# Optimization experiments

Hardware: AMD Instinct MI355X
Metric: run time of the kernel (lower is better)

## Reference

```python
import jax, jax.numpy as jnp
import numpy as np

N_NODES = 100000


def _graph_conv(x, W, b, src, dst, deg_out, deg_in, relu):
    # DGL GraphConv, norm='both':
    #   h = (x * D_out^{-1/2}) W ; agg = scatter_sum over edges ; out = agg * D_in^{-1/2} + b
    norm_src = jax.lax.rsqrt(jnp.maximum(deg_out, 1.0))  # [N]
    norm_dst = jax.lax.rsqrt(jnp.maximum(deg_in, 1.0))   # [N]
    h = (x * norm_src[:, None]) @ W                       # [N, d_out]
    agg = jax.ops.segment_sum(h[src], dst, num_segments=N_NODES)  # [N, d_out]
    out = agg * norm_dst[:, None] + b
    return jax.nn.relu(out) if relu else out


def setup_inputs() -> dict:
    key = jax.random.key(0)
    ks = jax.random.split(key, 8)
    E = 1600000
    in_dim, hid_dim, out_dim = 128, 128, 64
    feat = jax.random.normal(ks[0], (N_NODES, in_dim), dtype=jnp.float32)
    edge_index = jax.random.randint(ks[1], (2, E), 0, N_NODES, dtype=jnp.int64)
    s = 1.0 / np.sqrt(in_dim)
    sh = 1.0 / np.sqrt(hid_dim)
    return {
        "feat": feat,
        "edge_index": edge_index,
        "W0": jax.random.normal(ks[2], (in_dim, hid_dim), dtype=jnp.float32) * s,
        "b0": jnp.zeros((hid_dim,), dtype=jnp.float32),
        "W1": jax.random.normal(ks[3], (hid_dim, hid_dim), dtype=jnp.float32) * sh,
        "b1": jnp.zeros((hid_dim,), dtype=jnp.float32),
        "W2": jax.random.normal(ks[4], (hid_dim, out_dim), dtype=jnp.float32) * sh,
        "b2": jnp.zeros((out_dim,), dtype=jnp.float32),
    }


def reference(feat, edge_index, W0, b0, W1, b1, W2, b2):
    src, dst = edge_index[0], edge_index[1]
    ones = jnp.ones(src.shape, dtype=feat.dtype)
    deg_out = jax.ops.segment_sum(ones, src, num_segments=N_NODES)  # src out-degree
    deg_in = jax.ops.segment_sum(ones, dst, num_segments=N_NODES)   # dst in-degree
    h = _graph_conv(feat, W0, b0, src, dst, deg_out, deg_in, relu=True)
    h = _graph_conv(h, W1, b1, src, dst, deg_out, deg_in, relu=True)
    h = _graph_conv(h, W2, b2, src, dst, deg_out, deg_in, relu=False)
    return h
```

## Files before the change

kernel.cpp:

```cpp
#include <hip/hip_runtime.h>
#include <hip/hip_fp16.h>


typedef _Float16 h8 __attribute__((ext_vector_type(8)));
typedef float f32x4 __attribute__((ext_vector_type(4)));

#define HWORDS 25024
#define NHS 64
#define NHD 256

__global__ __launch_bounds__(1024) void k_pre(const int* __restrict__ src,
                                              const int* __restrict__ dst, int E,
                                              unsigned* __restrict__ histo_s,
                                              unsigned* __restrict__ histo_d,
                                              const float* __restrict__ W0,
                                              const float* __restrict__ W1,
                                              const float* __restrict__ W2,
                                              __half* __restrict__ Wt0,
                                              __half* __restrict__ Wt1,
                                              __half* __restrict__ Wt2) {
    __shared__ unsigned H[HWORDS];
    const int b = blockIdx.x;
    const int tid = threadIdx.x;
    if (b < NHS + NHD) {
        const bool isS = b < NHS;
        const int c = isS ? b : b - NHS;
        const int NC = isS ? NHS : NHD;
        const int* arr = isS ? src : dst;
        unsigned* outp = (isS ? histo_s : histo_d) + (size_t)c * HWORDS;
        for (int i = tid; i < HWORDS; i += 1024) H[i] = 0;
        __syncthreads();
        const int perB = ((E + NC - 1) / NC + 3) & ~3;
        const int e0 = min(c * perB, E), e1 = min(e0 + perB, E);
        int i = e0 + tid * 4;
        for (; i + 3 < e1; i += 4096) {
            int4 s4 = *(const int4*)(arr + i);
            atomicAdd(&H[s4.x >> 2], 1u << ((s4.x & 3) * 8));
            atomicAdd(&H[s4.y >> 2], 1u << ((s4.y & 3) * 8));
            atomicAdd(&H[s4.z >> 2], 1u << ((s4.z & 3) * 8));
            atomicAdd(&H[s4.w >> 2], 1u << ((s4.w & 3) * 8));
        }
        for (; i < e1; ++i) {
            int s = arr[i];
            atomicAdd(&H[s >> 2], 1u << ((s & 3) * 8));
        }
        __syncthreads();
        for (int i2 = tid; i2 < HWORDS; i2 += 1024) outp[i2] = H[i2];
    } else {
        for (int j = tid; j < 40960; j += 1024) {
            if (j < 16384) {
                int nn = j >> 7, k = j & 127;
                Wt0[j] = __float2half(W0[k * 128 + nn]);
            } else if (j < 32768) {
                int i2 = j - 16384;
                int nn = i2 >> 7, k = i2 & 127;
                Wt1[i2] = __float2half(W1[k * 128 + nn]);
            } else {
                int i2 = j - 32768;
                int nn = i2 >> 7, k = i2 & 127;
                Wt2[i2] = __float2half(W2[k * 64 + nn]);
            }
        }
    }
}

__global__ __launch_bounds__(256) void k_scan1(const unsigned* __restrict__ histo_s,
                                               unsigned* __restrict__ histo_d,
                                               int* __restrict__ rp,
                                               int* __restrict__ bsum,
                                               float* __restrict__ ns,
                                               float* __restrict__ nd, int n) {
    __shared__ unsigned qsd[4][64];
    __shared__ unsigned qss[4][64];
    __shared__ unsigned di4[64];
    __shared__ unsigned do4[64];
    const int tid = threadIdx.x, lane = tid & 63, q = tid >> 6;
    const int w = blockIdx.x * 64 + lane;
    {
        unsigned s = 0;
#pragma unroll 8
        for (int b = q * (NHD / 4); b < (q + 1) * (NHD / 4); ++b)
            s += histo_d[(size_t)b * HWORDS + w];
        qsd[q][lane] = s;
        unsigned s2 = 0;
#pragma unroll
        for (int b = q * (NHS / 4); b < (q + 1) * (NHS / 4); ++b)
            s2 += histo_s[(size_t)b * HWORDS + w];
        qss[q][lane] = s2;
    }
    __syncthreads();
    if (q == 0) {
        di4[lane] = qsd[0][lane] + qsd[1][lane] + qsd[2][lane] + qsd[3][lane];
        do4[lane] = qss[0][lane] + qss[1][lane] + qss[2][lane] + qss[3][lane];
    }
    {
        unsigned run = 0;
        for (int k = 0; k < q; ++k) run += qsd[k][lane];
#pragma unroll 8
        for (int b = q * (NHD / 4); b < (q + 1) * (NHD / 4); ++b) {
            unsigned c4 = histo_d[(size_t)b * HWORDS + w];
            histo_d[(size_t)b * HWORDS + w] = run;
            run += c4;
        }
    }
    __syncthreads();
    int i = blockIdx.x * 256 + tid;
    int v = 0;
    if (i < n) {
        int sh = (tid & 3) * 8;
        v = (di4[tid >> 2] >> sh) & 255;
        int dgo = (do4[tid >> 2] >> sh) & 255;
        nd[i] = rsqrtf((float)max(v, 1));
        ns[i] = rsqrtf((float)max(dgo, 1));
    }
    int x = v;
#pragma unroll
    for (int off = 1; off < 64; off <<= 1) {
        int t = __shfl_up(x, off, 64);
        if (lane >= off) x += t;
    }
    __shared__ int ws[4];
    if (lane == 63) ws[q] = x;
    __syncthreads();
    int wo = 0;
    for (int k = 0; k < q; ++k) wo += ws[k];
    int incl = wo + x;
    if (i < n) rp[i] = incl - v;
    if (tid == 255) bsum[blockIdx.x] = incl;
}

__global__ __launch_bounds__(512) void k_scan2(int* __restrict__ bsum, int nb,
                                               int* __restrict__ rpN) {
    __shared__ int s[512];
    const int tid = threadIdx.x;
    int v = (tid < nb) ? bsum[tid] : 0;
    s[tid] = v;
    __syncthreads();
    for (int off = 1; off < 512; off <<= 1) {
        int t = (tid >= off) ? s[tid - off] : 0;
        __syncthreads();
        s[tid] += t;
        __syncthreads();
    }
    if (tid < nb) bsum[tid] = s[tid] - v;
    if (tid == nb - 1) *rpN = v;
}

__global__ __launch_bounds__(1024) void k_scatter2(const int* __restrict__ src,
                                                   const int* __restrict__ dst, int E,
                                                   const int* __restrict__ rp,
                                                   const int* __restrict__ bsum,
                                                   const unsigned* __restrict__ pfx_all,
                                                   int* __restrict__ csr) {
    __shared__ unsigned Hd[HWORDS];
    const int tid = threadIdx.x;
    for (int i = tid; i < HWORDS; i += 1024) Hd[i] = 0;
    __syncthreads();
    const int c = blockIdx.x;
    const int perB = ((E + NHD - 1) / NHD + 3) & ~3;
    const int e0 = min(c * perB, E), e1 = min(e0 + perB, E);
    const unsigned* pfx = pfx_all + (size_t)c * HWORDS;
    int i = e0 + tid * 4;
    for (; i + 3 < e1; i += 4096) {
        int4 d4 = *(const int4*)(dst + i);
        int4 s4 = *(const int4*)(src + i);
#define PROC(dd, ss)                                                            \
        {                                                                       \
            int sh = ((dd) & 3) * 8;                                            \
            int base = rp[dd] + bsum[(dd) >> 8] +                               \
                       (int)((pfx[(dd) >> 2] >> sh) & 255u);                    \
            unsigned old = atomicAdd(&Hd[(dd) >> 2], 1u << sh);                 \
            csr[base + (int)((old >> sh) & 255u)] = (ss);                       \
        }
        PROC(d4.x, s4.x) PROC(d4.y, s4.y) PROC(d4.z, s4.z) PROC(d4.w, s4.w)
    }
    for (; i < e1; ++i) PROC(dst[i], src[i])
#undef PROC
}

template <int BN, bool F32A>
__device__ __forceinline__ void gemm_body(const void* __restrict__ Ap,
                                          const __half* __restrict__ Wt,
                                          __half* __restrict__ C, int n, int gb) {
    constexpr int K = 128, BM = 128, LDR = K + 8;
    __shared__ __half Al[BM * LDR];
    __shared__ __half Bl[BN * LDR];
    const int tid = threadIdx.x;
    const int row0 = gb * BM;
    if (F32A) {
        const float* A = (const float*)Ap;
#pragma unroll
        for (int q = 0; q < 16; ++q) {
            int fi = q * 256 + tid;
            int r = fi >> 5, c = (fi & 31) * 4;
            int gr = row0 + r;
            float4 v = make_float4(0.f, 0.f, 0.f, 0.f);
            if (gr < n) v = *(const float4*)(A + (size_t)gr * K + c);
            __half2 h0 = __floats2half2_rn(v.x, v.y);
            __half2 h1 = __floats2half2_rn(v.z, v.w);
            uint2 pk = make_uint2(*(unsigned*)&h0, *(unsigned*)&h1);
            *(uint2*)&Al[r * LDR + c] = pk;
        }
    } else {
        const __half* A = (const __half*)Ap;
#pragma unroll
        for (int q = 0; q < 8; ++q) {
            int fi = q * 256 + tid;
            int r = fi >> 4, c = (fi & 15) * 8;
            int gr = row0 + r;
            float4 v = make_float4(0.f, 0.f, 0.f, 0.f);
            if (gr < n) v = *(const float4*)(A + (size_t)gr * K + c);
            *(float4*)&Al[r * LDR + c] = v;
        }
    }
#pragma unroll
    for (int q = 0; q < BN / 16; ++q) {
        int fi = q * 256 + tid;
        int r = fi >> 4, c = (fi & 15) * 8;
        *(float4*)&Bl[r * LDR + c] = *(const float4*)(Wt + (size_t)r * K + c);
    }
    __syncthreads();
    const int wid = tid >> 6, lane = tid & 63;
    const int lo = lane & 15, hi = lane >> 4;
    constexpr int NC = BN / 16;
    f32x4 acc[2][NC];
#pragma unroll
    for (int t = 0; t < 2; ++t)
#pragma unroll
        for (int c = 0; c < NC; ++c) acc[t][c] = (f32x4){0.f, 0.f, 0.f, 0.f};
#pragma unroll
    for (int kc = 0; kc < 4; ++kc) {
        h8 aF[2];
#pragma unroll
        for (int t = 0; t < 2; ++t)
            aF[t] = *(const h8*)&Al[(32 * wid + 16 * t + lo) * LDR + 32 * kc + 8 * hi];
#pragma unroll
        for (int c = 0; c < NC; ++c) {
            h8 bF = *(const h8*)&Bl[(16 * c + lo) * LDR + 32 * kc + 8 * hi];
#pragma unroll
            for (int t = 0; t < 2; ++t)
                acc[t][c] = __builtin_amdgcn_mfma_f32_16x16x32_f16(aF[t], bF, acc[t][c], 0, 0, 0);
        }
    }
#pragma unroll
    for (int t = 0; t < 2; ++t) {
#pragma unroll
        for (int j = 0; j < 4; ++j) {
            int gr = row0 + 32 * wid + 16 * t + 4 * hi + j;
            if (gr < n) {
#pragma unroll
                for (int c = 0; c < NC; ++c)
                    C[(size_t)gr * BN + 16 * c + lo] = __float2half(acc[t][c][j]);
            }
        }
    }
}

template <int BN, bool F32A>
__global__ __launch_bounds__(256) void k_gemm(const void* __restrict__ A,
                                              const __half* __restrict__ Wt,
                                              __half* __restrict__ C, int n) {
    gemm_body<BN, F32A>(A, Wt, C, n, blockIdx.x);
}

template <bool RELU, bool SSCALE>
__global__ __launch_bounds__(256) void k_agg128h(const __half2* __restrict__ H,
                                                 const int* __restrict__ rp,
                                                 const int* __restrict__ bsum,
                                                 const int* __restrict__ cs,
                                                 const float* __restrict__ nd,
                                                 const float* __restrict__ ns,
                                                 const float* __restrict__ b,
                                                 __half2* __restrict__ out, int n) {
    const int wid = threadIdx.x >> 6, lane = threadIdx.x & 63;
    const int node = blockIdx.x * 4 + wid;
    if (node >= n) return;
    const int beg = rp[node] + bsum[node >> 8];
    const int end = rp[node + 1] + bsum[(node + 1) >> 8];
    float2 a0 = make_float2(0.f, 0.f), a1 = a0, a2 = a0, a3 = a0;
    float2 a4 = a0, a5 = a0, a6 = a0, a7 = a0;
    for (int e = beg; e < end; e += 8) {
        int s[8];
        float w[8];
#pragma unroll
        for (int j = 0; j < 8; ++j) {
            int idx = e + j;
            int r = (idx < end) ? idx : beg;
            r = __builtin_amdgcn_readfirstlane(r);
            s[j] = cs[r];
            w[j] = (idx < end) ? 1.f : 0.f;
        }
        if (SSCALE) {
#pragma unroll
            for (int j = 0; j < 8; ++j) w[j] *= ns[s[j]];
        }
        float2 v0 = __half22float2(H[(size_t)s[0] * 64 + lane]);
        float2 v1 = __half22float2(H[(size_t)s[1] * 64 + lane]);
        float2 v2 = __half22float2(H[(size_t)s[2] * 64 + lane]);
        float2 v3 = __half22float2(H[(size_t)s[3] * 64 + lane]);
        float2 v4 = __half22float2(H[(size_t)s[4] * 64 + lane]);
        float2 v5 = __half22float2(H[(size_t)s[5] * 64 + lane]);
        float2 v6 = __half22float2(H[(size_t)s[6] * 64 + lane]);
        float2 v7 = __half22float2(H[(size_t)s[7] * 64 + lane]);
        a0.x = fmaf(v0.x, w[0], a0.x); a0.y = fmaf(v0.y, w[0], a0.y);
        a1.x = fmaf(v1.x, w[1], a1.x); a1.y = fmaf(v1.y, w[1], a1.y);
        a2.x = fmaf(v2.x, w[2], a2.x); a2.y = fmaf(v2.y, w[2], a2.y);
        a3.x = fmaf(v3.x, w[3], a3.x); a3.y = fmaf(v3.y, w[3], a3.y);
        a4.x = fmaf(v4.x, w[4], a4.x); a4.y = fmaf(v4.y, w[4], a4.y);
        a5.x = fmaf(v5.x, w[5], a5.x); a5.y = fmaf(v5.y, w[5], a5.y);
        a6.x = fmaf(v6.x, w[6], a6.x); a6.y = fmaf(v6.y, w[6], a6.y);
        a7.x = fmaf(v7.x, w[7], a7.x); a7.y = fmaf(v7.y, w[7], a7.y);
    }
    const float sc = nd[node];
    const float sn = ns[node];
    float2 bb = ((const float2*)b)[lane];
    float ax = ((a0.x + a1.x) + (a2.x + a3.x)) + ((a4.x + a5.x) + (a6.x + a7.x));
    float ay = ((a0.y + a1.y) + (a2.y + a3.y)) + ((a4.y + a5.y) + (a6.y + a7.y));
    float ox = ax * sc + bb.x;
    float oy = ay * sc + bb.y;
    if (RELU) { ox = fmaxf(ox, 0.f); oy = fmaxf(oy, 0.f); }
    ox *= sn; oy *= sn;
    out[(size_t)node * 64 + lane] = __floats2half2_rn(ox, oy);
}

__global__ __launch_bounds__(256) void k_agg64h(const __half* __restrict__ H,
                                                const int* __restrict__ rp,
                                                const int* __restrict__ bsum,
                                                const int* __restrict__ cs,
                                                const float* __restrict__ nd,
                                                const float* __restrict__ b,
                                                float* __restrict__ out, int n) {
    const int wid = threadIdx.x >> 6, lane = threadIdx.x & 63;
    const int node = blockIdx.x * 4 + wid;
    if (node >= n) return;
    const int beg = rp[node] + bsum[node >> 8];
    const int end = rp[node + 1] + bsum[(node + 1) >> 8];
    float a0 = 0.f, a1 = 0.f, a2 = 0.f, a3 = 0.f;
    float a4 = 0.f, a5 = 0.f, a6 = 0.f, a7 = 0.f;
    for (int e = beg; e < end; e += 8) {
        int s[8];
        float w[8];
#pragma unroll
        for (int j = 0; j < 8; ++j) {
            int idx = e + j;
            int r = (idx < end) ? idx : beg;
            r = __builtin_amdgcn_readfirstlane(r);
            s[j] = cs[r];
            w[j] = (idx < end) ? 1.f : 0.f;
        }
        a0 = fmaf(__half2float(H[(size_t)s[0] * 64 + lane]), w[0], a0);
        a1 = fmaf(__half2float(H[(size_t)s[1] * 64 + lane]), w[1], a1);
        a2 = fmaf(__half2float(H[(size_t)s[2] * 64 + lane]), w[2], a2);
        a3 = fmaf(__half2float(H[(size_t)s[3] * 64 + lane]), w[3], a3);
        a4 = fmaf(__half2float(H[(size_t)s[4] * 64 + lane]), w[4], a4);
        a5 = fmaf(__half2float(H[(size_t)s[5] * 64 + lane]), w[5], a5);
        a6 = fmaf(__half2float(H[(size_t)s[6] * 64 + lane]), w[6], a6);
        a7 = fmaf(__half2float(H[(size_t)s[7] * 64 + lane]), w[7], a7);
    }
    float a = ((a0 + a1) + (a2 + a3)) + ((a4 + a5) + (a6 + a7));
    out[(size_t)node * 64 + lane] = a * nd[node] + b[lane];
}

extern "C" void kernel_launch(void* const* d_in, const int* in_sizes, int n_in,
                              void* d_out, int out_size, void* d_ws, size_t ws_size,
                              hipStream_t stream) {
    const float* feat = (const float*)d_in[0];
    const int* ei = (const int*)d_in[1];
    const float* W0 = (const float*)d_in[2];
    const float* b0 = (const float*)d_in[3];
    const float* W1 = (const float*)d_in[4];
    const float* b1 = (const float*)d_in[5];
    const float* W2 = (const float*)d_in[6];
    const float* b2 = (const float*)d_in[7];
    float* out = (float*)d_out;

    const int N = in_sizes[0] / 128;
    const int E = in_sizes[1] / 2;
    const int* src = ei;
    const int* dst = ei + E;
    const int NB = (N + 255) / 256;

    char* w = (char*)d_ws;
    float* norm_src = (float*)w; w += (size_t)N * 4;
    float* norm_dst = (float*)w; w += (size_t)N * 4;
    unsigned* histo_s = (unsigned*)w; w += (size_t)NHS * HWORDS * 4;
    unsigned* histo_d = (unsigned*)w; w += (size_t)NHD * HWORDS * 4;
    int* rp    = (int*)w;        w += ((size_t)(N + 1) * 4 + 15) / 16 * 16;
    int* bsum  = (int*)w;        w += 512 * 4;
    int* csr   = (int*)w;        w += (size_t)E * 4;
    __half* Wt0 = (__half*)w;    w += 128 * 128 * 2;
    __half* Wt1 = (__half*)w;    w += 128 * 128 * 2;
    __half* Wt2 = (__half*)w;    w += 128 * 64 * 2;
    __half* Hb = (__half*)w;     w += (size_t)N * 128 * 2;
    __half* Xb = (__half*)w;     w += (size_t)N * 128 * 2;

    const int GB = (N + 127) / 128;
    const int agg_grid = (N + 3) / 4;

    k_pre<<<NHS + NHD + 1, 1024, 0, stream>>>(src, dst, E, histo_s, histo_d,
                                              W0, W1, W2, Wt0, Wt1, Wt2);
    k_scan1<<<NB, 256, 0, stream>>>(histo_s, histo_d, rp, bsum, norm_src, norm_dst, N);
    k_scan2<<<1, 512, 0, stream>>>(bsum, NB, rp + N);
    k_scatter2<<<NHD, 1024, 0, stream>>>(src, dst, E, rp, bsum, histo_d, csr);

    k_gemm<128, true><<<GB, 256, 0, stream>>>(feat, Wt0, Hb, N);
    k_agg128h<true, true><<<agg_grid, 256, 0, stream>>>((const __half2*)Hb, rp, bsum, csr,
                                                        norm_dst, norm_src, b0, (__half2*)Xb, N);
    k_gemm<128, false><<<GB, 256, 0, stream>>>(Xb, Wt1, Hb, N);
    k_agg128h<true, false><<<agg_grid, 256, 0, stream>>>((const __half2*)Hb, rp, bsum, csr,
                                                         norm_dst, norm_src, b1, (__half2*)Xb, N);
    k_gemm<64, false><<<GB, 256, 0, stream>>>(Xb, Wt2, Hb, N);
    k_agg64h<<<agg_grid, 256, 0, stream>>>(Hb, rp, bsum, csr, norm_dst, b2, out, N);
}
```

Baseline: 348.8 us.

## Record in-bucket positions during histogram; fuse CSR scatter with first GEMM

The dst histogram pass now saves each edge's per-chunk slot (the atomic's old count) into a byte array. The CSR scatter then only reads that slot instead of redoing the shared-memory histogram and atomics, so it no longer needs its large LDS buffer and runs with 256-thread blocks. Those scatter blocks are launched in the same grid as the first-layer GEMM blocks, which overlaps two independent kernels and removes one launch. The cost is an extra E-byte write and read of the position array, plus a mixed kernel whose two block types have different resource profiles.

```diff
diff --git a/kernel.cpp b/kernel.cpp
--- a/kernel.cpp
+++ b/kernel.cpp
@@ -13,6 +13,7 @@
                                               const int* __restrict__ dst, int E,
                                               unsigned* __restrict__ histo_s,
                                               unsigned* __restrict__ histo_d,
+                                              unsigned char* __restrict__ pos,
                                               const float* __restrict__ W0,
                                               const float* __restrict__ W1,
                                               const float* __restrict__ W2,
@@ -22,27 +23,52 @@
     __shared__ unsigned H[HWORDS];
     const int b = blockIdx.x;
     const int tid = threadIdx.x;
-    if (b < NHS + NHD) {
-        const bool isS = b < NHS;
-        const int c = isS ? b : b - NHS;
-        const int NC = isS ? NHS : NHD;
-        const int* arr = isS ? src : dst;
-        unsigned* outp = (isS ? histo_s : histo_d) + (size_t)c * HWORDS;
+    if (b < NHS) {
+        const int c = b;
+        unsigned* outp = histo_s + (size_t)c * HWORDS;
         for (int i = tid; i < HWORDS; i += 1024) H[i] = 0;
         __syncthreads();
-        const int perB = ((E + NC - 1) / NC + 3) & ~3;
+        const int perB = ((E + NHS - 1) / NHS + 3) & ~3;
         const int e0 = min(c * perB, E), e1 = min(e0 + perB, E);
         int i = e0 + tid * 4;
         for (; i + 3 < e1; i += 4096) {
-            int4 s4 = *(const int4*)(arr + i);
+            int4 s4 = *(const int4*)(src + i);
             atomicAdd(&H[s4.x >> 2], 1u << ((s4.x & 3) * 8));
             atomicAdd(&H[s4.y >> 2], 1u << ((s4.y & 3) * 8));
             atomicAdd(&H[s4.z >> 2], 1u << ((s4.z & 3) * 8));
             atomicAdd(&H[s4.w >> 2], 1u << ((s4.w & 3) * 8));
         }
         for (; i < e1; ++i) {
-            int s = arr[i];
+            int s = src[i];
             atomicAdd(&H[s >> 2], 1u << ((s & 3) * 8));
+        }
+        __syncthreads();
+        for (int i2 = tid; i2 < HWORDS; i2 += 1024) outp[i2] = H[i2];
+    } else if (b < NHS + NHD) {
+        const int c = b - NHS;
+        unsigned* outp = histo_d + (size_t)c * HWORDS;
+        for (int i = tid; i < HWORDS; i += 1024) H[i] = 0;
+        __syncthreads();
+        const int perB = ((E + NHD - 1) / NHD + 3) & ~3;
+        const int e0 = min(c * perB, E), e1 = min(e0 + perB, E);
+        int i = e0 + tid * 4;
+        for (; i + 3 < e1; i += 4096) {
+            int4 d4 = *(const int4*)(dst + i);
+            unsigned o0 = atomicAdd(&H[d4.x >> 2], 1u << ((d4.x & 3) * 8));
+            unsigned o1 = atomicAdd(&H[d4.y >> 2], 1u << ((d4.y & 3) * 8));
+            unsigned o2 = atomicAdd(&H[d4.z >> 2], 1u << ((d4.z & 3) * 8));
+            unsigned o3 = atomicAdd(&H[d4.w >> 2], 1u << ((d4.w & 3) * 8));
+            uchar4 p4;
+            p4.x = (unsigned char)((o0 >> ((d4.x & 3) * 8)) & 255u);
+            p4.y = (unsigned char)((o1 >> ((d4.y & 3) * 8)) & 255u);
+            p4.z = (unsigned char)((o2 >> ((d4.z & 3) * 8)) & 255u);
+            p4.w = (unsigned char)((o3 >> ((d4.w & 3) * 8)) & 255u);
+            *(uchar4*)(pos + i) = p4;
+        }
+        for (; i < e1; ++i) {
+            int d = dst[i];
+            unsigned o = atomicAdd(&H[d >> 2], 1u << ((d & 3) * 8));
+            pos[i] = (unsigned char)((o >> ((d & 3) * 8)) & 255u);
         }
         __syncthreads();
         for (int i2 = tid; i2 < HWORDS; i2 += 1024) outp[i2] = H[i2];
@@ -146,38 +172,6 @@
     if (tid == nb - 1) *rpN = v;
 }
 
-__global__ __launch_bounds__(1024) void k_scatter2(const int* __restrict__ src,
-                                                   const int* __restrict__ dst, int E,
-                                                   const int* __restrict__ rp,
-                                                   const int* __restrict__ bsum,
-                                                   const unsigned* __restrict__ pfx_all,
-                                                   int* __restrict__ csr) {
-    __shared__ unsigned Hd[HWORDS];
-    const int tid = threadIdx.x;
-    for (int i = tid; i < HWORDS; i += 1024) Hd[i] = 0;
-    __syncthreads();
-    const int c = blockIdx.x;
-    const int perB = ((E + NHD - 1) / NHD + 3) & ~3;
-    const int e0 = min(c * perB, E), e1 = min(e0 + perB, E);
-    const unsigned* pfx = pfx_all + (size_t)c * HWORDS;
-    int i = e0 + tid * 4;
-    for (; i + 3 < e1; i += 4096) {
-        int4 d4 = *(const int4*)(dst + i);
-        int4 s4 = *(const int4*)(src + i);
-#define PROC(dd, ss)                                                            \
-        {                                                                       \
-            int sh = ((dd) & 3) * 8;                                            \
-            int base = rp[dd] + bsum[(dd) >> 8] +                               \
-                       (int)((pfx[(dd) >> 2] >> sh) & 255u);                    \
-            unsigned old = atomicAdd(&Hd[(dd) >> 2], 1u << sh);                 \
-            csr[base + (int)((old >> sh) & 255u)] = (ss);                       \
-        }
-        PROC(d4.x, s4.x) PROC(d4.y, s4.y) PROC(d4.z, s4.z) PROC(d4.w, s4.w)
-    }
-    for (; i < e1; ++i) PROC(dst[i], src[i])
-#undef PROC
-}
-
 template <int BN, bool F32A>
 __device__ __forceinline__ void gemm_body(const void* __restrict__ Ap,
                                           const __half* __restrict__ Wt,
@@ -253,6 +247,42 @@
                     C[(size_t)gr * BN + 16 * c + lo] = __float2half(acc[t][c][j]);
             }
         }
+    }
+}
+
+__global__ __launch_bounds__(256) void k_s3g0(const int* __restrict__ src,
+                                              const int* __restrict__ dst, int E,
+                                              const int* __restrict__ rp,
+                                              const int* __restrict__ bsum,
+                                              const unsigned* __restrict__ pfx_all,
+                                              const unsigned char* __restrict__ pos,
+                                              int* __restrict__ csr,
+                                              const float* __restrict__ feat,
+                                              const __half* __restrict__ Wt0,
+                                              __half* __restrict__ Hb, int n) {
+    const int b = blockIdx.x;
+    if (b < NHD) {
+        const int perB = ((E + NHD - 1) / NHD + 3) & ~3;
+        const int e0 = min(b * perB, E), e1 = min(e0 + perB, E);
+        const unsigned* pfx = pfx_all + (size_t)b * HWORDS;
+        int i = e0 + threadIdx.x * 4;
+        for (; i + 3 < e1; i += 1024) {
+            int4 d4 = *(const int4*)(dst + i);
+            int4 s4 = *(const int4*)(src + i);
+            uchar4 p4 = *(const uchar4*)(pos + i);
+#define PLACE(dd, ss, pp)                                                       \
+            {                                                                   \
+                int sh = ((dd) & 3) * 8;                                        \
+                csr[rp[dd] + bsum[(dd) >> 8] +                                  \
+                    (int)((pfx[(dd) >> 2] >> sh) & 255u) + (int)(pp)] = (ss);   \
+            }
+            PLACE(d4.x, s4.x, p4.x) PLACE(d4.y, s4.y, p4.y)
+            PLACE(d4.z, s4.z, p4.z) PLACE(d4.w, s4.w, p4.w)
+        }
+        for (; i < e1; ++i) PLACE(dst[i], src[i], pos[i])
+#undef PLACE
+    } else {
+        gemm_body<128, true>(feat, Wt0, Hb, n, b - NHD);
     }
 }
 
@@ -388,6 +418,7 @@
     int* rp    = (int*)w;        w += ((size_t)(N + 1) * 4 + 15) / 16 * 16;
     int* bsum  = (int*)w;        w += 512 * 4;
     int* csr   = (int*)w;        w += (size_t)E * 4;
+    unsigned char* pos = (unsigned char*)w; w += ((size_t)E + 15) / 16 * 16;
     __half* Wt0 = (__half*)w;    w += 128 * 128 * 2;
     __half* Wt1 = (__half*)w;    w += 128 * 128 * 2;
     __half* Wt2 = (__half*)w;    w += 128 * 64 * 2;
@@ -397,13 +428,13 @@
     const int GB = (N + 127) / 128;
     const int agg_grid = (N + 3) / 4;
 
-    k_pre<<<NHS + NHD + 1, 1024, 0, stream>>>(src, dst, E, histo_s, histo_d,
+    k_pre<<<NHS + NHD + 1, 1024, 0, stream>>>(src, dst, E, histo_s, histo_d, pos,
                                               W0, W1, W2, Wt0, Wt1, Wt2);
     k_scan1<<<NB, 256, 0, stream>>>(histo_s, histo_d, rp, bsum, norm_src, norm_dst, N);
     k_scan2<<<1, 512, 0, stream>>>(bsum, NB, rp + N);
-    k_scatter2<<<NHD, 1024, 0, stream>>>(src, dst, E, rp, bsum, histo_d, csr);
-
-    k_gemm<128, true><<<GB, 256, 0, stream>>>(feat, Wt0, Hb, N);
+    k_s3g0<<<NHD + GB, 256, 0, stream>>>(src, dst, E, rp, bsum, histo_d, pos, csr,
+                                         feat, Wt0, Hb, N);
+
     k_agg128h<true, true><<<agg_grid, 256, 0, stream>>>((const __half2*)Hb, rp, bsum, csr,
                                                         norm_dst, norm_src, b0, (__half2*)Xb, N);
     k_gemm<128, false><<<GB, 256, 0, stream>>>(Xb, Wt1, Hb, N);
```

Measured after the change: 346.4 us. No clear change (-0.7%).
